# Performance work log

Hardware: AMD Instinct MI355X
Metric: run time of the kernel (lower is better)

Reference implementation:

```python
import jax, jax.numpy as jnp
import numpy as np

B, S, HID = 1, 2048, 4096
NH, NKV, HD = 32, 8, 128
GROUPS = NH // NKV
ROPE_THETA = 10000.0


def rotate_half(x):
    x1, x2 = jnp.split(x, 2, axis=-1)
    return jnp.concatenate([-x2, x1], axis=-1)


def rope_cos_sin(position_ids, head_dim, dtype):
    # inv_freq: [hd/2]; position_ids: [B, S]
    inv_freq = 1.0 / (ROPE_THETA ** (jnp.arange(0, head_dim, 2, dtype=jnp.float32) / head_dim))
    freqs = position_ids.astype(jnp.float32)[..., None] * inv_freq  # [B, S, hd/2]
    emb = jnp.concatenate([freqs, freqs], axis=-1)                  # [B, S, hd]
    return jnp.cos(emb).astype(dtype), jnp.sin(emb).astype(dtype)


def apply_rope(x, cos, sin):
    # x: [B, H, S, hd]; cos/sin: [B, S, hd] -> broadcast over heads
    return x * cos[:, None] + rotate_half(x) * sin[:, None]


def setup_inputs() -> dict:
    key = jax.random.key(0)
    ks = jax.random.split(key, 5)
    scale = 0.02
    return {
        "hidden_states": jax.random.normal(ks[0], (B, S, HID), dtype=jnp.float32),
        "wq": jax.random.normal(ks[1], (HID, NH * HD), dtype=jnp.float32) * scale,
        "wk": jax.random.normal(ks[2], (HID, NKV * HD), dtype=jnp.float32) * scale,
        "wv": jax.random.normal(ks[3], (HID, NKV * HD), dtype=jnp.float32) * scale,
        "wo": jax.random.normal(ks[4], (NH * HD, HID), dtype=jnp.float32) * scale,
        "position_ids": jnp.arange(S, dtype=jnp.int32)[None, :],
    }


def reference(hidden_states, wq, wk, wv, wo, position_ids):
    bsz, q_len, _ = hidden_states.shape
    # projections (nn.Linear, bias=False)
    q = (hidden_states @ wq).reshape(bsz, q_len, NH, HD).transpose(0, 2, 1, 3)   # [B,NH,S,hd]
    k = (hidden_states @ wk).reshape(bsz, q_len, NKV, HD).transpose(0, 2, 1, 3)  # [B,NKV,S,hd]
    v = (hidden_states @ wv).reshape(bsz, q_len, NKV, HD).transpose(0, 2, 1, 3)
    # RoPE applied to Q and K at global positions (prefill: no past cache)
    cos, sin = rope_cos_sin(position_ids, HD, q.dtype)
    q = apply_rope(q, cos, sin)
    k = apply_rope(k, cos, sin)
    # GQA: expand KV heads to query heads
    k_full = jnp.repeat(k, GROUPS, axis=1)  # [B,NH,S,hd]
    v_full = jnp.repeat(v, GROUPS, axis=1)
    # prefill flash attention == causal SDPA
    logits = jnp.einsum('bhqd,bhkd->bhqk', q, k_full) / jnp.sqrt(jnp.asarray(HD, q.dtype))
    causal = jnp.tril(jnp.ones((q_len, q_len), dtype=bool))
    neg = jnp.asarray(jnp.finfo(q.dtype).min, q.dtype)
    logits = jnp.where(causal[None, None], logits, neg)
    probs = jax.nn.softmax(logits, axis=-1)                     # [B,NH,S,S]
    attn = jnp.einsum('bhqk,bhkd->bhqd', probs, v_full)          # [B,NH,S,hd]
    attn_output = attn.transpose(0, 2, 1, 3).reshape(bsz, q_len, NH * HD) @ wo
    # chunked prefill eviction scores: causal attention probs accumulated over
    # all queries, aggregated per KV head group -> [B, NKV, kv_len]
    accumulated_scores = probs.sum(axis=2).reshape(bsz, NKV, GROUPS, q_len).sum(axis=2)
    return attn_output, accumulated_scores
```

## Files before the change

kernel.cpp:

```cpp
#include <hip/hip_runtime.h>
#include <hip/hip_bf16.h>
#include <cstdint>
#include <cstddef>

#define S_LEN 2048
#define HID_DIM 4096
#define NH 32
#define NKV 8
#define HD 128
#define LOG2E 1.4426950408889634f
#define SCALE 0.08838834764831845f

typedef __attribute__((ext_vector_type(8))) short bf16x8;
typedef __attribute__((ext_vector_type(4))) float f32x4;
typedef __attribute__((ext_vector_type(4))) short short4v;
typedef __attribute__((ext_vector_type(4))) unsigned u32x4;

__device__ __forceinline__ short f2bf(float f) {
  union { float f; unsigned u; } v; v.f = f;
  return (short)((v.u + 0x7fffu + ((v.u >> 16) & 1u)) >> 16);
}
__device__ __forceinline__ float bf2f(short s) {
  union { unsigned u; float f; } v; v.u = ((unsigned)(unsigned short)s) << 16;
  return v.f;
}
__device__ __forceinline__ unsigned cvt_pk_bf16(float lo, float hi) {
  unsigned r;
  asm("v_cvt_pk_bf16_f32 %0, %1, %2" : "=v"(r) : "v"(lo), "v"(hi));
  return r;
}
__device__ __forceinline__ void gld_lds16(const void* g, void* l) {
  __builtin_amdgcn_global_load_lds((const __attribute__((address_space(1))) unsigned*)g,
                                   (__attribute__((address_space(3))) unsigned*)l, 16, 0, 0);
}

#define WAITVM4() asm volatile("s_waitcnt vmcnt(4)" ::: "memory")
#define WAITVM2() asm volatile("s_waitcnt vmcnt(2)" ::: "memory")
#define WAITVM0() asm volatile("s_waitcnt vmcnt(0)" ::: "memory")

__global__ void cvt_kernel(const float* __restrict__ in, short* __restrict__ out, int n) {
  int i = (blockIdx.x * 256 + threadIdx.x) * 4;
  if (i < n) {
    float4 f = *(const float4*)(in + i);
    short4v o = { f2bf(f.x), f2bf(f.y), f2bf(f.z), f2bf(f.w) };
    *(short4v*)(out + i) = o;
  }
}

__global__ void tconv_kernel(const float* __restrict__ in, short* __restrict__ out, int R, int C) {
  __shared__ float tile[32][33];
  int tr = blockIdx.y * 32, tc = blockIdx.x * 32;
  int tx = threadIdx.x & 31, ty = threadIdx.x >> 5;
#pragma unroll
  for (int i = 0; i < 32; i += 8)
    tile[ty + i][tx] = in[(size_t)(tr + ty + i) * C + tc + tx];
  __syncthreads();
#pragma unroll
  for (int i = 0; i < 32; i += 8)
    out[(size_t)(tc + ty + i) * R + tr + tx] = f2bf(tile[tx][ty + i]);
}

template<int MODE>
__global__ __launch_bounds__(256, 4) void gemm_bt_kernel(
    const short* __restrict__ A, const short* __restrict__ Bt,
    void* __restrict__ Cout, int M, int N, int K, int rchunk, int cchunk)
{
  __shared__ short As[2][128 * 32];
  __shared__ short Bs[2][128 * 32];
  const int tid = threadIdx.x;
  const int lane = tid & 63;
  const int w = tid >> 6;
  const int wm = w >> 1, wn = w & 1;
  const int xcd = blockIdx.x & 7;
  const int local = blockIdx.x >> 3;
  const int by = (xcd >> 2) * rchunk + (local % rchunk);
  const int bx = (xcd & 3) * cchunk + (local / rchunk);
  const int m0 = by * 128, n0 = bx * 128;

  auto stage = [&](int bb, int k0) {
#pragma unroll
    for (int rep = 0; rep < 2; rep++) {
      int c = rep * 256 + tid;
      int row = c >> 2, slot = c & 3;
      int gs = slot ^ (row & 3);
      gld_lds16(A + (size_t)(m0 + row) * K + k0 + gs * 8, &As[bb][c * 8]);
      gld_lds16(Bt + (size_t)(n0 + row) * K + k0 + gs * 8, &Bs[bb][c * 8]);
    }
  };

  f32x4 acc[4][4];
#pragma unroll
  for (int i = 0; i < 4; i++)
#pragma unroll
    for (int j = 0; j < 4; j++) acc[i][j] = (f32x4){0.f, 0.f, 0.f, 0.f};

  const int NT = K >> 5;
  stage(0, 0);
  for (int kt = 0; kt < NT; kt++) {
    const int b = kt & 1;
    if (kt + 1 < NT) { stage(b ^ 1, (kt + 1) << 5); WAITVM4(); }
    else             { WAITVM0(); }
    __builtin_amdgcn_s_barrier();

    bf16x8 af[4], bf[4];
#pragma unroll
    for (int ms = 0; ms < 4; ms++) {
      int row = wm * 64 + ms * 16 + (lane & 15);
      af[ms] = *(const bf16x8*)(&As[b][row * 32 + (((lane >> 4) ^ (row & 3)) << 3)]);
    }
#pragma unroll
    for (int ns = 0; ns < 4; ns++) {
      int row = wn * 64 + ns * 16 + (lane & 15);
      bf[ns] = *(const bf16x8*)(&Bs[b][row * 32 + (((lane >> 4) ^ (row & 3)) << 3)]);
    }
#pragma unroll
    for (int ms = 0; ms < 4; ms++)
#pragma unroll
      for (int ns = 0; ns < 4; ns++)
        acc[ms][ns] = __builtin_amdgcn_mfma_f32_16x16x32_bf16(af[ms], bf[ns], acc[ms][ns], 0, 0, 0);

    __builtin_amdgcn_s_barrier();
  }

#pragma unroll
  for (int ms = 0; ms < 4; ms++) {
    int mb = m0 + wm * 64 + ms * 16 + ((lane >> 4) << 2);
#pragma unroll
    for (int ns = 0; ns < 4; ns++) {
      int n = n0 + wn * 64 + ns * 16 + (lane & 15);
      if (MODE == 3) {
        short* o = (short*)Cout;
        if (n < NH * HD) {
          int head = n >> 7, d = n & 127;
#pragma unroll
          for (int r = 0; r < 4; r++)
            o[((size_t)head * M + (mb + r)) * HD + d] = f2bf(acc[ms][ns][r]);
        } else if (n < (NH + NKV) * HD) {
          int head = (n - NH * HD) >> 7, d = n & 127;
          short* ok = o + (size_t)NH * S_LEN * HD;
#pragma unroll
          for (int r = 0; r < 4; r++)
            ok[((size_t)head * M + (mb + r)) * HD + d] = f2bf(acc[ms][ns][r]);
        } else {
          int head = (n - (NH + NKV) * HD) >> 7, d = n & 127;
          short* ov = o + (size_t)(NH + NKV) * S_LEN * HD;
          short4v pk;
#pragma unroll
          for (int r = 0; r < 4; r++) pk[r] = f2bf(acc[ms][ns][r]);
          *(short4v*)(ov + ((size_t)head * HD + d) * M + mb) = pk;
        }
      } else {
        float* o = (float*)Cout;
#pragma unroll
        for (int r = 0; r < 4; r++)
          o[(size_t)(mb + r) * N + n] = acc[ms][ns][r];
      }
    }
  }
}

__global__ void rope_kernel(short* __restrict__ q, short* __restrict__ k,
                            const int* __restrict__ pos_ids) {
  const int s = blockIdx.x;
  const int hh = blockIdx.y * 4 + threadIdx.y;
  const int d = threadIdx.x;
  const float pos = (float)pos_ids[s];
  const float inv = __expf(-(float)d * 0.14391157f);
  float sn, c;
  __sincosf(pos * inv, &sn, &c);
  short* base = (hh < NH) ? (q + ((size_t)hh * S_LEN + s) * HD)
                          : (k + ((size_t)(hh - NH) * S_LEN + s) * HD);
  float x1 = bf2f(base[d]), x2 = bf2f(base[d + 64]);
  base[d] = f2bf(x1 * c - x2 * sn);
  base[d + 64] = f2bf(x2 * c + x1 * sn);
}

__global__ __launch_bounds__(512, 2) void attn_kernel(
    const short* __restrict__ Qr, const short* __restrict__ Kr, const short* __restrict__ Vt,
    short* __restrict__ attn_out, float* __restrict__ scores)
{
  __shared__ short Ks[2][64 * 128];
  __shared__ short Vs[2][128 * 64];
  __shared__ float cs[2048];

  const int tid = threadIdx.x;
  const int lane = tid & 63;
  const int w = tid >> 6;
  const int hi = lane >> 4;
  const int ql = lane & 15;
  const int lin = (blockIdx.x & 7) * 32 + (blockIdx.x >> 3);
  const int h = lin >> 3;
  const int pr = lin & 7;
  const int kvh = h >> 2;
  const float CS = SCALE * LOG2E;

  const short* KrB = Kr + (size_t)kvh * S_LEN * HD;
  const short* VtB = Vt + (size_t)kvh * HD * S_LEN;

  for (int i = tid; i < 2048; i += 512) cs[i] = 0.f;

  auto stageKV = [&](int bb, int t) {
    const int kb2 = t * 64;
#pragma unroll
    for (int rep = 0; rep < 2; rep++) {
      int c = rep * 512 + tid;
      int x = c >> 4, slot = c & 15;
      int key = (x & 32) | ((x & 16) >> 2) | ((x & 12) << 1) | (x & 3);
      int gs = slot ^ (x & 7);
      gld_lds16(KrB + (size_t)(kb2 + key) * HD + gs * 8, &Ks[bb][c * 8]);
    }
#pragma unroll
    for (int rep = 0; rep < 2; rep++) {
      int c = rep * 512 + tid;
      int d = c >> 3, slot = c & 7;
      int gs = slot ^ (d & 7);
      gld_lds16(VtB + (size_t)d * S_LEN + kb2 + gs * 8, &Vs[bb][c * 8]);
    }
  };
  auto stageK = [&](int bb, int t) {
    const int kb2 = t * 64;
#pragma unroll
    for (int rep = 0; rep < 2; rep++) {
      int c = rep * 512 + tid;
      int x = c >> 4, slot = c & 15;
      int key = (x & 32) | ((x & 16) >> 2) | ((x & 12) << 1) | (x & 3);
      int gs = slot ^ (x & 7);
      gld_lds16(KrB + (size_t)(kb2 + key) * HD + gs * 8, &Ks[bb][c * 8]);
    }
  };

  int maxnt = 0;

  for (int sidx = 0; sidx < 2; sidx++) {
    const int qt = sidx ? (15 - pr) : pr;
    const int nt = 2 * qt + 2;
    if (nt > maxnt) maxnt = nt;
    const int qbase = qt * 128 + w * 16;
    const int qglob = qbase + ql;
    const int qmax = qbase + 15;

    bf16x8 qf[4];
    {
      const short* qrow = Qr + ((size_t)h * S_LEN + qglob) * HD + hi * 8;
#pragma unroll
      for (int kc = 0; kc < 4; kc++) qf[kc] = *(const bf16x8*)(qrow + kc * 32);
    }

    f32x4 oacc[8];
#pragma unroll
    for (int i = 0; i < 8; i++) oacc[i] = (f32x4){0.f, 0.f, 0.f, 0.f};
    float lsum = 0.f;

    stageKV(0, 0);
    for (int t = 0; t < nt; t++) {
      const int b = t & 1;
      const int kb = t * 64;
      if (t + 1 < nt) { stageKV(b ^ 1, t + 1); WAITVM4(); }
      else            { WAITVM0(); }
      __builtin_amdgcn_s_barrier();

      if (kb <= qmax) {
        f32x4 sf[4];
#pragma unroll
        for (int g = 0; g < 4; g++) sf[g] = (f32x4){0.f, 0.f, 0.f, 0.f};
        __builtin_amdgcn_s_setprio(1);
#pragma unroll
        for (int g = 0; g < 4; g++)
#pragma unroll
          for (int kc = 0; kc < 4; kc++) {
            int row = g * 16 + ql;
            bf16x8 kf = *(const bf16x8*)(&Ks[b][row * 128 + (((kc * 4 + hi) ^ (ql & 7)) << 3)]);
            sf[g] = __builtin_amdgcn_mfma_f32_16x16x32_bf16(kf, qf[kc], sf[g], 0, 0, 0);
          }
        __builtin_amdgcn_s_setprio(0);

        float p[4][4];
#pragma unroll
        for (int g = 0; g < 4; g++)
#pragma unroll
          for (int r = 0; r < 4; r++) p[g][r] = exp2f(sf[g][r] * CS);
        if (kb + 63 > qbase) {
#pragma unroll
          for (int g = 0; g < 4; g++)
#pragma unroll
            for (int r = 0; r < 4; r++) {
              int key = kb + ((g >> 1) << 5) + ((g & 1) << 2) + (hi << 3) + r;
              if (key > qglob) p[g][r] = 0.f;
            }
        }
#pragma unroll
        for (int g = 0; g < 4; g++)
#pragma unroll
          for (int r = 0; r < 4; r++) lsum += p[g][r];

        bf16x8 pa[2];
#pragma unroll
        for (int kh = 0; kh < 2; kh++) {
          u32x4 pw;
          pw[0] = cvt_pk_bf16(p[2 * kh][0], p[2 * kh][1]);
          pw[1] = cvt_pk_bf16(p[2 * kh][2], p[2 * kh][3]);
          pw[2] = cvt_pk_bf16(p[2 * kh + 1][0], p[2 * kh + 1][1]);
          pw[3] = cvt_pk_bf16(p[2 * kh + 1][2], p[2 * kh + 1][3]);
          pa[kh] = __builtin_bit_cast(bf16x8, pw);
        }

        __builtin_amdgcn_s_setprio(1);
#pragma unroll
        for (int ds = 0; ds < 8; ds++) {
          int d = ds * 16 + ql;
#pragma unroll
          for (int kh = 0; kh < 2; kh++) {
            bf16x8 vf = *(const bf16x8*)(&Vs[b][d * 64 + (((kh * 4 + hi) ^ (d & 7)) << 3)]);
            oacc[ds] = __builtin_amdgcn_mfma_f32_16x16x32_bf16(pa[kh], vf, oacc[ds], 0, 0, 0);
          }
        }
        __builtin_amdgcn_s_setprio(0);
      }
      __builtin_amdgcn_s_barrier();
    }

    lsum += __shfl_xor(lsum, 16);
    lsum += __shfl_xor(lsum, 32);
    float rl[4];
#pragma unroll
    for (int r = 0; r < 4; r++) rl[r] = 1.f / __shfl(lsum, hi * 4 + r);

#pragma unroll
    for (int ds = 0; ds < 8; ds++)
#pragma unroll
      for (int r = 0; r < 4; r++) {
        int qq = qbase + hi * 4 + r;
        int d = ds * 16 + ql;
        attn_out[(size_t)qq * HID_DIM + h * HD + d] = f2bf(oacc[ds][r] * rl[r]);
      }

    stageK(0, 0);
    for (int t = 0; t < nt; t++) {
      const int b = t & 1;
      const int kb = t * 64;
      if (t + 1 < nt) { stageK(b ^ 1, t + 1); WAITVM2(); }
      else            { WAITVM0(); }
      __builtin_amdgcn_s_barrier();

      if (kb <= qmax) {
        f32x4 sg[4];
#pragma unroll
        for (int c = 0; c < 4; c++) sg[c] = (f32x4){0.f, 0.f, 0.f, 0.f};
        __builtin_amdgcn_s_setprio(1);
#pragma unroll
        for (int c = 0; c < 4; c++)
#pragma unroll
          for (int kc = 0; kc < 4; kc++) {
            int row = c * 16 + ql;
            bf16x8 kf = *(const bf16x8*)(&Ks[b][row * 128 + (((kc * 4 + hi) ^ (ql & 7)) << 3)]);
            sg[c] = __builtin_amdgcn_mfma_f32_16x16x32_bf16(qf[kc], kf, sg[c], 0, 0, 0);
          }
        __builtin_amdgcn_s_setprio(0);

        const bool diag = (kb + 63 > qbase);
#pragma unroll
        for (int c = 0; c < 4; c++) {
          int key = kb + ((c >> 1) << 5) + ((c & 1) << 2) + ((ql >> 2) << 3) + (ql & 3);
          float sum = 0.f;
          if (diag) {
#pragma unroll
            for (int r = 0; r < 4; r++) {
              float pv = exp2f(sg[c][r] * CS) * rl[r];
              if (key > qbase + hi * 4 + r) pv = 0.f;
              sum += pv;
            }
          } else {
#pragma unroll
            for (int r = 0; r < 4; r++) sum += exp2f(sg[c][r] * CS) * rl[r];
          }
          sum += __shfl_xor(sum, 16);
          sum += __shfl_xor(sum, 32);
          if (lane < 16) atomicAdd(&cs[key], sum);
        }
      }
      __builtin_amdgcn_s_barrier();
    }
  }

  __builtin_amdgcn_s_barrier();
  const int nk = maxnt * 64;
  for (int i = tid; i < nk; i += 512)
    atomicAdd(scores + (size_t)kvh * S_LEN + i, cs[i]);
}

extern "C" void kernel_launch(void* const* d_in, const int* in_sizes, int n_in,
                              void* d_out, int out_size, void* d_ws, size_t ws_size,
                              hipStream_t stream) {
  const float* hs = (const float*)d_in[0];
  const float* wq = (const float*)d_in[1];
  const float* wk = (const float*)d_in[2];
  const float* wv = (const float*)d_in[3];
  const float* wo = (const float*)d_in[4];
  const int* pos = (const int*)d_in[5];
  float* out = (float*)d_out;

  char* ws = (char*)d_ws;
  const size_t off_hs   = 0;
  const size_t off_wqT  = off_hs   + (size_t)S_LEN * HID_DIM * 2;
  const size_t off_wkT  = off_wqT  + (size_t)HID_DIM * HID_DIM * 2;
  const size_t off_wvT  = off_wkT  + (size_t)1024 * HID_DIM * 2;
  const size_t off_woT  = off_wvT  + (size_t)1024 * HID_DIM * 2;
  const size_t off_Qr   = off_woT  + (size_t)HID_DIM * HID_DIM * 2;
  const size_t off_Kr   = off_Qr   + (size_t)NH * S_LEN * HD * 2;
  const size_t off_Vt   = off_Kr   + (size_t)NKV * S_LEN * HD * 2;
  const size_t off_attn = off_Vt   + (size_t)NKV * HD * S_LEN * 2;

  short* hsb  = (short*)(ws + off_hs);
  short* wqT  = (short*)(ws + off_wqT);
  short* wkT  = (short*)(ws + off_wkT);
  short* wvT  = (short*)(ws + off_wvT);
  short* woT  = (short*)(ws + off_woT);
  short* Qr   = (short*)(ws + off_Qr);
  short* Kr   = (short*)(ws + off_Kr);
  short* Vt   = (short*)(ws + off_Vt);
  short* attb = (short*)(ws + off_attn);

  cvt_kernel<<<dim3((S_LEN * HID_DIM) / 1024), 256, 0, stream>>>(hs, hsb, S_LEN * HID_DIM);
  tconv_kernel<<<dim3(128, 128), 256, 0, stream>>>(wq, wqT, HID_DIM, HID_DIM);
  tconv_kernel<<<dim3(32, 128), 256, 0, stream>>>(wk, wkT, HID_DIM, 1024);
  tconv_kernel<<<dim3(32, 128), 256, 0, stream>>>(wv, wvT, HID_DIM, 1024);
  tconv_kernel<<<dim3(128, 128), 256, 0, stream>>>(wo, woT, HID_DIM, HID_DIM);

  gemm_bt_kernel<3><<<768, 256, 0, stream>>>(hsb, wqT, Qr, S_LEN, 6144, HID_DIM, 8, 12);

  rope_kernel<<<dim3(S_LEN, 10), dim3(64, 4), 0, stream>>>(Qr, Kr, pos);

  hipMemsetAsync(out + (size_t)S_LEN * HID_DIM, 0, (size_t)NKV * S_LEN * sizeof(float), stream);
  attn_kernel<<<256, 512, 0, stream>>>(Qr, Kr, Vt, attb, out + (size_t)S_LEN * HID_DIM);

  gemm_bt_kernel<2><<<512, 256, 0, stream>>>(attb, woT, out, S_LEN, HID_DIM, HID_DIM, 8, 8);
}
```

Baseline: 386.7 us.

## Switch attention kernel to 32x32x16 MFMA with 4 waves of 32 queries

Result: slower. 405.5 us (+4.9%).

```diff
diff --git a/kernel.cpp b/kernel.cpp
--- a/kernel.cpp
+++ b/kernel.cpp
@@ -13,6 +13,7 @@
 
 typedef __attribute__((ext_vector_type(8))) short bf16x8;
 typedef __attribute__((ext_vector_type(4))) float f32x4;
+typedef __attribute__((ext_vector_type(16))) float f32x16;
 typedef __attribute__((ext_vector_type(4))) short short4v;
 typedef __attribute__((ext_vector_type(4))) unsigned u32x4;
 
@@ -34,8 +35,8 @@
                                    (__attribute__((address_space(3))) unsigned*)l, 16, 0, 0);
 }
 
+#define WAITVM8() asm volatile("s_waitcnt vmcnt(8)" ::: "memory")
 #define WAITVM4() asm volatile("s_waitcnt vmcnt(4)" ::: "memory")
-#define WAITVM2() asm volatile("s_waitcnt vmcnt(2)" ::: "memory")
 #define WAITVM0() asm volatile("s_waitcnt vmcnt(0)" ::: "memory")
 
 __global__ void cvt_kernel(const float* __restrict__ in, short* __restrict__ out, int n) {
@@ -175,7 +176,7 @@
   base[d + 64] = f2bf(x2 * c + x1 * sn);
 }
 
-__global__ __launch_bounds__(512, 2) void attn_kernel(
+__global__ __launch_bounds__(256, 2) void attn_kernel(
     const short* __restrict__ Qr, const short* __restrict__ Kr, const short* __restrict__ Vt,
     short* __restrict__ attn_out, float* __restrict__ scores)
 {
@@ -186,8 +187,8 @@
   const int tid = threadIdx.x;
   const int lane = tid & 63;
   const int w = tid >> 6;
-  const int hi = lane >> 4;
-  const int ql = lane & 15;
+  const int h2 = lane >> 5;
+  const int l31 = lane & 31;
   const int lin = (blockIdx.x & 7) * 32 + (blockIdx.x >> 3);
   const int h = lin >> 3;
   const int pr = lin & 7;
@@ -197,194 +198,179 @@
   const short* KrB = Kr + (size_t)kvh * S_LEN * HD;
   const short* VtB = Vt + (size_t)kvh * HD * S_LEN;
 
-  for (int i = tid; i < 2048; i += 512) cs[i] = 0.f;
-
-  auto stageKV = [&](int bb, int t) {
+  for (int i = tid; i < 2048; i += 256) cs[i] = 0.f;
+
+  auto stageK = [&](int bb, int t) {
     const int kb2 = t * 64;
 #pragma unroll
-    for (int rep = 0; rep < 2; rep++) {
-      int c = rep * 512 + tid;
+    for (int rep = 0; rep < 4; rep++) {
+      int c = rep * 256 + tid;
       int x = c >> 4, slot = c & 15;
-      int key = (x & 32) | ((x & 16) >> 2) | ((x & 12) << 1) | (x & 3);
+      int key = (x & 0x33) | ((x & 4) << 1) | ((x & 8) >> 1);
       int gs = slot ^ (x & 7);
       gld_lds16(KrB + (size_t)(kb2 + key) * HD + gs * 8, &Ks[bb][c * 8]);
     }
-#pragma unroll
-    for (int rep = 0; rep < 2; rep++) {
-      int c = rep * 512 + tid;
+  };
+  auto stageV = [&](int bb, int t) {
+    const int kb2 = t * 64;
+#pragma unroll
+    for (int rep = 0; rep < 4; rep++) {
+      int c = rep * 256 + tid;
       int d = c >> 3, slot = c & 7;
       int gs = slot ^ (d & 7);
       gld_lds16(VtB + (size_t)d * S_LEN + kb2 + gs * 8, &Vs[bb][c * 8]);
     }
   };
-  auto stageK = [&](int bb, int t) {
-    const int kb2 = t * 64;
-#pragma unroll
-    for (int rep = 0; rep < 2; rep++) {
-      int c = rep * 512 + tid;
-      int x = c >> 4, slot = c & 15;
-      int key = (x & 32) | ((x & 16) >> 2) | ((x & 12) << 1) | (x & 3);
-      int gs = slot ^ (x & 7);
-      gld_lds16(KrB + (size_t)(kb2 + key) * HD + gs * 8, &Ks[bb][c * 8]);
-    }
-  };
-
-  int maxnt = 0;
+
+  const int maxnt = 2 * (15 - pr) + 2;
 
   for (int sidx = 0; sidx < 2; sidx++) {
     const int qt = sidx ? (15 - pr) : pr;
     const int nt = 2 * qt + 2;
-    if (nt > maxnt) maxnt = nt;
-    const int qbase = qt * 128 + w * 16;
-    const int qglob = qbase + ql;
-    const int qmax = qbase + 15;
-
-    bf16x8 qf[4];
+    const int qbase = qt * 128 + w * 32;
+    const int qglob = qbase + l31;
+    const int qmaxw = qbase + 31;
+
+    bf16x8 qf[8];
     {
-      const short* qrow = Qr + ((size_t)h * S_LEN + qglob) * HD + hi * 8;
-#pragma unroll
-      for (int kc = 0; kc < 4; kc++) qf[kc] = *(const bf16x8*)(qrow + kc * 32);
-    }
-
-    f32x4 oacc[8];
-#pragma unroll
-    for (int i = 0; i < 8; i++) oacc[i] = (f32x4){0.f, 0.f, 0.f, 0.f};
+      const short* qrow = Qr + ((size_t)h * S_LEN + qglob) * HD + h2 * 8;
+#pragma unroll
+      for (int kc = 0; kc < 8; kc++) qf[kc] = *(const bf16x8*)(qrow + kc * 16);
+    }
+
+    f32x16 oacc[4];
+#pragma unroll
+    for (int i = 0; i < 4; i++) oacc[i] = (f32x16)(0.f);
     float lsum = 0.f;
 
-    stageKV(0, 0);
+    stageK(0, 0); stageV(0, 0);
     for (int t = 0; t < nt; t++) {
       const int b = t & 1;
       const int kb = t * 64;
-      if (t + 1 < nt) { stageKV(b ^ 1, t + 1); WAITVM4(); }
+      if (t + 1 < nt) { stageK(b ^ 1, t + 1); stageV(b ^ 1, t + 1); WAITVM8(); }
       else            { WAITVM0(); }
       __builtin_amdgcn_s_barrier();
 
-      if (kb <= qmax) {
-        f32x4 sf[4];
-#pragma unroll
-        for (int g = 0; g < 4; g++) sf[g] = (f32x4){0.f, 0.f, 0.f, 0.f};
+      if (kb <= qmaxw) {
+        f32x16 sf[2];
+        sf[0] = (f32x16)(0.f); sf[1] = (f32x16)(0.f);
         __builtin_amdgcn_s_setprio(1);
 #pragma unroll
-        for (int g = 0; g < 4; g++)
-#pragma unroll
-          for (int kc = 0; kc < 4; kc++) {
-            int row = g * 16 + ql;
-            bf16x8 kf = *(const bf16x8*)(&Ks[b][row * 128 + (((kc * 4 + hi) ^ (ql & 7)) << 3)]);
-            sf[g] = __builtin_amdgcn_mfma_f32_16x16x32_bf16(kf, qf[kc], sf[g], 0, 0, 0);
+        for (int kc = 0; kc < 8; kc++)
+#pragma unroll
+          for (int bl = 0; bl < 2; bl++) {
+            int x = bl * 32 + l31;
+            bf16x8 kf = *(const bf16x8*)(&Ks[b][x * 128 + (((kc * 2 + h2) ^ (lane & 7)) << 3)]);
+            sf[bl] = __builtin_amdgcn_mfma_f32_32x32x16_bf16(kf, qf[kc], sf[bl], 0, 0, 0);
           }
         __builtin_amdgcn_s_setprio(0);
 
-        float p[4][4];
-#pragma unroll
-        for (int g = 0; g < 4; g++)
-#pragma unroll
-          for (int r = 0; r < 4; r++) p[g][r] = exp2f(sf[g][r] * CS);
-        if (kb + 63 > qbase) {
-#pragma unroll
-          for (int g = 0; g < 4; g++)
-#pragma unroll
-            for (int r = 0; r < 4; r++) {
-              int key = kb + ((g >> 1) << 5) + ((g & 1) << 2) + (hi << 3) + r;
-              if (key > qglob) p[g][r] = 0.f;
+        float p[2][16];
+        const bool diag = (kb + 63 > qbase);
+#pragma unroll
+        for (int bl = 0; bl < 2; bl++)
+#pragma unroll
+          for (int a = 0; a < 4; a++)
+#pragma unroll
+            for (int cc = 0; cc < 4; cc++) {
+              float pv = exp2f(sf[bl][a * 4 + cc] * CS);
+              if (diag) {
+                int key = kb + bl * 32 + (a >> 1) * 16 + h2 * 8 + (a & 1) * 4 + cc;
+                if (key > qglob) pv = 0.f;
+              }
+              p[bl][a * 4 + cc] = pv;
+              lsum += pv;
             }
+
+        bf16x8 pa[4];
+#pragma unroll
+        for (int s = 0; s < 4; s++) {
+          const int bl = s >> 1, base = 8 * (s & 1);
+          u32x4 pw;
+          pw[0] = cvt_pk_bf16(p[bl][base + 0], p[bl][base + 1]);
+          pw[1] = cvt_pk_bf16(p[bl][base + 2], p[bl][base + 3]);
+          pw[2] = cvt_pk_bf16(p[bl][base + 4], p[bl][base + 5]);
+          pw[3] = cvt_pk_bf16(p[bl][base + 6], p[bl][base + 7]);
+          pa[s] = __builtin_bit_cast(bf16x8, pw);
         }
-#pragma unroll
-        for (int g = 0; g < 4; g++)
-#pragma unroll
-          for (int r = 0; r < 4; r++) lsum += p[g][r];
-
-        bf16x8 pa[2];
-#pragma unroll
-        for (int kh = 0; kh < 2; kh++) {
-          u32x4 pw;
-          pw[0] = cvt_pk_bf16(p[2 * kh][0], p[2 * kh][1]);
-          pw[1] = cvt_pk_bf16(p[2 * kh][2], p[2 * kh][3]);
-          pw[2] = cvt_pk_bf16(p[2 * kh + 1][0], p[2 * kh + 1][1]);
-          pw[3] = cvt_pk_bf16(p[2 * kh + 1][2], p[2 * kh + 1][3]);
-          pa[kh] = __builtin_bit_cast(bf16x8, pw);
-        }
 
         __builtin_amdgcn_s_setprio(1);
 #pragma unroll
-        for (int ds = 0; ds < 8; ds++) {
-          int d = ds * 16 + ql;
-#pragma unroll
-          for (int kh = 0; kh < 2; kh++) {
-            bf16x8 vf = *(const bf16x8*)(&Vs[b][d * 64 + (((kh * 4 + hi) ^ (d & 7)) << 3)]);
-            oacc[ds] = __builtin_amdgcn_mfma_f32_16x16x32_bf16(pa[kh], vf, oacc[ds], 0, 0, 0);
+        for (int s = 0; s < 4; s++)
+#pragma unroll
+          for (int db = 0; db < 4; db++) {
+            int d = db * 32 + l31;
+            bf16x8 vf = *(const bf16x8*)(&Vs[b][d * 64 + (((s * 2 + h2) ^ (lane & 7)) << 3)]);
+            oacc[db] = __builtin_amdgcn_mfma_f32_32x32x16_bf16(pa[s], vf, oacc[db], 0, 0, 0);
           }
-        }
         __builtin_amdgcn_s_setprio(0);
       }
       __builtin_amdgcn_s_barrier();
     }
 
-    lsum += __shfl_xor(lsum, 16);
     lsum += __shfl_xor(lsum, 32);
-    float rl[4];
-#pragma unroll
-    for (int r = 0; r < 4; r++) rl[r] = 1.f / __shfl(lsum, hi * 4 + r);
-
-#pragma unroll
-    for (int ds = 0; ds < 8; ds++)
-#pragma unroll
-      for (int r = 0; r < 4; r++) {
-        int qq = qbase + hi * 4 + r;
-        int d = ds * 16 + ql;
-        attn_out[(size_t)qq * HID_DIM + h * HD + d] = f2bf(oacc[ds][r] * rl[r]);
+    float rlv = 1.f / lsum;
+    float rl16[16];
+#pragma unroll
+    for (int r = 0; r < 16; r++)
+      rl16[r] = __shfl(rlv, (r & 3) + 8 * (r >> 2) + 4 * h2);
+
+#pragma unroll
+    for (int db = 0; db < 4; db++) {
+      int d = db * 32 + l31;
+#pragma unroll
+      for (int r = 0; r < 16; r++) {
+        int qq = qbase + (r & 3) + 8 * (r >> 2) + 4 * h2;
+        attn_out[(size_t)qq * HID_DIM + h * HD + d] = f2bf(oacc[db][r] * rl16[r]);
       }
-
+    }
+
+    const int xl = (l31 & 0x13) | ((l31 & 4) << 1) | ((l31 & 8) >> 1);
     stageK(0, 0);
     for (int t = 0; t < nt; t++) {
       const int b = t & 1;
       const int kb = t * 64;
-      if (t + 1 < nt) { stageK(b ^ 1, t + 1); WAITVM2(); }
+      if (t + 1 < nt) { stageK(b ^ 1, t + 1); WAITVM4(); }
       else            { WAITVM0(); }
       __builtin_amdgcn_s_barrier();
 
-      if (kb <= qmax) {
-        f32x4 sg[4];
-#pragma unroll
-        for (int c = 0; c < 4; c++) sg[c] = (f32x4){0.f, 0.f, 0.f, 0.f};
+      if (kb <= qmaxw) {
+        f32x16 sg[2];
+        sg[0] = (f32x16)(0.f); sg[1] = (f32x16)(0.f);
         __builtin_amdgcn_s_setprio(1);
 #pragma unroll
-        for (int c = 0; c < 4; c++)
-#pragma unroll
-          for (int kc = 0; kc < 4; kc++) {
-            int row = c * 16 + ql;
-            bf16x8 kf = *(const bf16x8*)(&Ks[b][row * 128 + (((kc * 4 + hi) ^ (ql & 7)) << 3)]);
-            sg[c] = __builtin_amdgcn_mfma_f32_16x16x32_bf16(qf[kc], kf, sg[c], 0, 0, 0);
+        for (int kc = 0; kc < 8; kc++)
+#pragma unroll
+          for (int bl = 0; bl < 2; bl++) {
+            int x = bl * 32 + xl;
+            bf16x8 kf = *(const bf16x8*)(&Ks[b][x * 128 + (((kc * 2 + h2) ^ (x & 7)) << 3)]);
+            sg[bl] = __builtin_amdgcn_mfma_f32_32x32x16_bf16(qf[kc], kf, sg[bl], 0, 0, 0);
           }
         __builtin_amdgcn_s_setprio(0);
 
         const bool diag = (kb + 63 > qbase);
 #pragma unroll
-        for (int c = 0; c < 4; c++) {
-          int key = kb + ((c >> 1) << 5) + ((c & 1) << 2) + ((ql >> 2) << 3) + (ql & 3);
+        for (int bl = 0; bl < 2; bl++) {
+          int key = kb + bl * 32 + l31;
           float sum = 0.f;
-          if (diag) {
-#pragma unroll
-            for (int r = 0; r < 4; r++) {
-              float pv = exp2f(sg[c][r] * CS) * rl[r];
-              if (key > qbase + hi * 4 + r) pv = 0.f;
-              sum += pv;
-            }
-          } else {
-#pragma unroll
-            for (int r = 0; r < 4; r++) sum += exp2f(sg[c][r] * CS) * rl[r];
+#pragma unroll
+          for (int r = 0; r < 16; r++) {
+            float pv = exp2f(sg[bl][r] * CS) * rl16[r];
+            if (diag && key > qbase + (r & 3) + 8 * (r >> 2) + 4 * h2) pv = 0.f;
+            sum += pv;
           }
-          sum += __shfl_xor(sum, 16);
           sum += __shfl_xor(sum, 32);
-          if (lane < 16) atomicAdd(&cs[key], sum);
+          if (lane < 32) atomicAdd(&cs[key], sum);
         }
       }
       __builtin_amdgcn_s_barrier();
     }
   }
 
+  asm volatile("s_waitcnt lgkmcnt(0)" ::: "memory");
   __builtin_amdgcn_s_barrier();
   const int nk = maxnt * 64;
-  for (int i = tid; i < nk; i += 512)
+  for (int i = tid; i < nk; i += 256)
     atomicAdd(scores + (size_t)kvh * S_LEN + i, cs[i]);
 }
 
@@ -431,7 +417,7 @@
   rope_kernel<<<dim3(S_LEN, 10), dim3(64, 4), 0, stream>>>(Qr, Kr, pos);
 
   hipMemsetAsync(out + (size_t)S_LEN * HID_DIM, 0, (size_t)NKV * S_LEN * sizeof(float), stream);
-  attn_kernel<<<256, 512, 0, stream>>>(Qr, Kr, Vt, attb, out + (size_t)S_LEN * HID_DIM);
+  attn_kernel<<<256, 256, 0, stream>>>(Qr, Kr, Vt, attb, out + (size_t)S_LEN * HID_DIM);
 
   gemm_bt_kernel<2><<<512, 256, 0, stream>>>(attb, woT, out, S_LEN, HID_DIM, HID_DIM, 8, 8);
 }
```
